# Kernel optimization log

Hardware: AMD Instinct MI355X
Metric: run time of the kernel (lower is better)

The kernel has to match this reference:

```python
import jax, jax.numpy as jnp
import numpy as np
import math

D_MODEL = 1024
NUM_HEADS = 16
HEAD_DIM = D_MODEL // NUM_HEADS


def setup_inputs() -> dict:
    key = jax.random.key(0)
    ks = jax.random.split(key, 10)
    B, Sq, Skv = 2, 2048, 2048
    s = 1.0 / math.sqrt(D_MODEL)
    return {
        "X": jax.random.normal(ks[0], (B, Skv, D_MODEL), jnp.float32),
        "y": jax.random.normal(ks[1], (B, Sq, D_MODEL), jnp.float32),
        "qW": jax.random.normal(ks[2], (D_MODEL, D_MODEL), jnp.float32) * s,
        "qB": jnp.zeros((D_MODEL,), jnp.float32),
        "kW": jax.random.normal(ks[3], (D_MODEL, D_MODEL), jnp.float32) * s,
        "kB": jnp.zeros((D_MODEL,), jnp.float32),
        "vW": jax.random.normal(ks[4], (D_MODEL, D_MODEL), jnp.float32) * s,
        "vB": jnp.zeros((D_MODEL,), jnp.float32),
        "oW": jax.random.normal(ks[5], (D_MODEL, D_MODEL), jnp.float32) * s,
        "oB": jnp.zeros((D_MODEL,), jnp.float32),
    }


def _split_heads(x):
    # (B, S, D) -> (B, H, S, dk)
    B, S, _ = x.shape
    return x.reshape(B, S, NUM_HEADS, HEAD_DIM).transpose(0, 2, 1, 3)


def reference(X, y, qW, qB, kW, kB, vW, vB, oW, oB):
    B = X.shape[0]
    q = _split_heads(y @ qW + qB)   # queries come from y (decoder)
    k = _split_heads(X @ kW + kB)   # keys/values from X (encoder)
    v = _split_heads(X @ vW + vB)
    scale = 1.0 / math.sqrt(HEAD_DIM)
    scores = jnp.einsum("bhqd,bhkd->bhqk", q, k) * scale
    weights = jax.nn.softmax(scores, axis=-1)
    attn = jnp.einsum("bhqk,bhkd->bhqd", weights, v)
    concat = attn.transpose(0, 2, 1, 3).reshape(B, -1, D_MODEL)
    return concat @ oW + oB
```

## Files before the change

kernel.cpp:

```cpp
#include <hip/hip_runtime.h>
#include <hip/hip_bf16.h>
#include <math.h>

typedef __hip_bfloat16 bf16;
typedef __bf16 nbf16;
typedef __bf16 bf16x8 __attribute__((ext_vector_type(8)));
typedef __bf16 bf16x4 __attribute__((ext_vector_type(4)));
typedef float f32x4 __attribute__((ext_vector_type(4)));

#define D_MODEL 1024
#define NHEAD   16
#define HDK     64
#define BATCH   2
#define SEQ     2048
#define QSZ     ((size_t)BATCH * SEQ * D_MODEL)
#define WSZ     ((size_t)D_MODEL * D_MODEL)

__global__ void detect_dtype(const unsigned short* __restrict__ x, int* flag) {
    __shared__ int cnt;
    if (threadIdx.x == 0) cnt = 0;
    __syncthreads();
    int local = 0;
    for (int i = threadIdx.x; i < 4096; i += 256) {
        const unsigned short v = x[i];
        const int e = (v >> 7) & 0xFF;
        if (v == 0 || (e >= 96 && e <= 141)) local++;
    }
    atomicAdd(&cnt, local);
    __syncthreads();
    if (threadIdx.x == 0) *flag = (cnt >= 3600) ? 1 : 0;
}

__device__ __forceinline__ float ldIn(const void* p, size_t i, int isbf16) {
    return isbf16 ? __bfloat162float(((const bf16*)p)[i])
                  : ((const float*)p)[i];
}

__device__ __forceinline__ void gload_lds16(const void* g, void* l) {
    __builtin_amdgcn_global_load_lds(
        (const __attribute__((address_space(1))) void*)g,
        (__attribute__((address_space(3))) void*)l, 16, 0, 0);
}

__global__ void tobf16_xy(const void* __restrict__ X, const void* __restrict__ Y,
                          nbf16* __restrict__ Xb, nbf16* __restrict__ Yb,
                          const int* __restrict__ flagp) {
    const int flag = *flagp;
    const int half = (int)(QSZ / 2048);
    const bool isX = blockIdx.x < half;
    const void* in = isX ? X : Y;
    nbf16* out     = isX ? Xb : Yb;
    const size_t i = ((size_t)(isX ? blockIdx.x : blockIdx.x - half) * 256 +
                      threadIdx.x) * 8;
    if (flag) {
        *(uint4*)(out + i) = *(const uint4*)((const nbf16*)in + i);
    } else {
        const float4 a = *(const float4*)((const float*)in + i);
        const float4 b = *(const float4*)((const float*)in + i + 4);
        bf16x8 v = {(nbf16)a.x, (nbf16)a.y, (nbf16)a.z, (nbf16)a.w,
                    (nbf16)b.x, (nbf16)b.y, (nbf16)b.z, (nbf16)b.w};
        *(bf16x8*)(out + i) = v;
    }
}

__global__ void wtrans4(const void* __restrict__ qW, const void* __restrict__ kW,
                        const void* __restrict__ vW, const void* __restrict__ oW,
                        nbf16* __restrict__ Wt3, nbf16* __restrict__ Wto,
                        const int* __restrict__ flagp) {
    const int flag = *flagp;
    const int z = blockIdx.z;
    const void* W = (z == 0) ? qW : (z == 1) ? kW : (z == 2) ? vW : oW;
    nbf16* Wt = (z == 3) ? Wto : Wt3 + (size_t)z * WSZ;

    __shared__ float T[64][65];
    const int k0 = blockIdx.x * 64, n0 = blockIdx.y * 64;
    #pragma unroll
    for (int i = 0; i < 16; ++i) {
        const int idx = threadIdx.x + i * 256;
        const int r = idx >> 6, c = idx & 63;
        T[r][c] = ldIn(W, (size_t)(k0 + r) * D_MODEL + n0 + c, flag);
    }
    __syncthreads();
    #pragma unroll
    for (int i = 0; i < 16; ++i) {
        const int idx = threadIdx.x + i * 256;
        const int n = idx >> 6, k = idx & 63;
        Wt[(size_t)(n0 + n) * D_MODEL + k0 + k] = (nbf16)T[k][n];
    }
}

#define STAGE128(Albuf, Blbuf, Aptr, Bptr, t)                                  \
{                                                                              \
    const int _k0 = (t) * 64;                                                  \
    _Pragma("unroll")                                                          \
    for (int i = 0; i < 4; ++i) {                                              \
        const int row = i * 32 + wid * 8 + (lane >> 3);                        \
        const int ss  = (lane & 7) ^ (row & 7);                                \
        gload_lds16((Aptr) + (size_t)row * D_MODEL + _k0 + ss * 8,             \
                    (nbf16*)(Albuf) + i * 2048 + wid * 512);                   \
        gload_lds16((Bptr) + (size_t)row * D_MODEL + _k0 + ss * 8,             \
                    (nbf16*)(Blbuf) + i * 2048 + wid * 512);                   \
    }                                                                          \
}

#define GEMM128_LOOP(Al, Bl)                                                   \
    const int NT = D_MODEL / 64;                                               \
    for (int t = 0; t < NT; ++t) {                                             \
        const int cur = t & 1;                                                 \
        if (t + 1 < NT)                                                        \
            STAGE128(&Al[cur ^ 1][0][0], &Bl[cur ^ 1][0][0], Am, Bm, t + 1);   \
        _Pragma("unroll")                                                      \
        for (int kk = 0; kk < 2; ++kk) {                                       \
            bf16x8 af[4], bfr[4];                                              \
            _Pragma("unroll")                                                  \
            for (int mi = 0; mi < 4; ++mi) {                                   \
                const int ar = wr * 64 + mi * 16 + l15;                        \
                const int sl = ((kk << 2) + lg) ^ (ar & 7);                    \
                af[mi] = *(const bf16x8*)((const nbf16*)&Al[cur][ar][0] + sl * 8); \
            }                                                                  \
            _Pragma("unroll")                                                  \
            for (int ni = 0; ni < 4; ++ni) {                                   \
                const int br = wc * 64 + ni * 16 + l15;                        \
                const int sl = ((kk << 2) + lg) ^ (br & 7);                    \
                bfr[ni] = *(const bf16x8*)((const nbf16*)&Bl[cur][br][0] + sl * 8); \
            }                                                                  \
            _Pragma("unroll")                                                  \
            for (int mi = 0; mi < 4; ++mi)                                     \
                _Pragma("unroll")                                              \
                for (int ni = 0; ni < 4; ++ni)                                 \
                    acc[mi][ni] = __builtin_amdgcn_mfma_f32_16x16x32_bf16(     \
                        af[mi], bfr[ni], acc[mi][ni], 0, 0, 0);                \
        }                                                                      \
        __syncthreads();                                                       \
    }

__global__ __launch_bounds__(256, 2) void proj_qkv(
        const nbf16* __restrict__ Xb, const nbf16* __restrict__ Yb,
        const nbf16* __restrict__ Wt3,
        const void* __restrict__ qB, const void* __restrict__ kB,
        const void* __restrict__ vB,
        nbf16* __restrict__ outq, const int* __restrict__ flagp) {
    __shared__ nbf16 Al[2][128][64];
    __shared__ nbf16 Bl[2][128][64];

    const int flag = *flagp;
    const int tid  = threadIdx.x;
    const int wid  = tid >> 6;
    const int lane = tid & 63;
    const int l15  = lane & 15;
    const int lg   = lane >> 4;
    const int wr   = wid >> 1;
    const int wc   = wid & 1;

    const int id = blockIdx.x;
    const int sw = (id & 7) * 96 + (id >> 3);
    const int m0  = (sw & 31) * 128;
    const int ng0 = (sw >> 5) * 128;

    const nbf16* A  = (ng0 < D_MODEL) ? Yb : Xb;
    const nbf16* Bm = Wt3 + (size_t)ng0 * D_MODEL;
    const nbf16* Am = A + (size_t)m0 * D_MODEL;

    f32x4 acc[4][4];
    #pragma unroll
    for (int mi = 0; mi < 4; ++mi)
        #pragma unroll
        for (int ni = 0; ni < 4; ++ni) acc[mi][ni] = (f32x4){0.f, 0.f, 0.f, 0.f};

    STAGE128(&Al[0][0][0], &Bl[0][0][0], Am, Bm, 0);
    __syncthreads();

    GEMM128_LOOP(Al, Bl)

    #pragma unroll
    for (int ni = 0; ni < 4; ++ni) {
        const int n  = ng0 + wc * 64 + ni * 16 + l15;
        const int wh = n >> 10;
        const int nl = n & 1023;
        const void* bp = (wh == 0) ? qB : (wh == 1) ? kB : vB;
        const float bias = ldIn(bp, (size_t)nl, flag);
        nbf16* outp = outq + (size_t)wh * QSZ;
        #pragma unroll
        for (int mi = 0; mi < 4; ++mi) {
            #pragma unroll
            for (int r = 0; r < 4; ++r) {
                const int m = m0 + wr * 64 + mi * 16 + lg * 4 + r;
                const float v = acc[mi][ni][r] + bias;
                const int b = m >> 11, s = m & (SEQ - 1);
                const int h = nl >> 6,  d = nl & (HDK - 1);
                outp[(((size_t)(b * NHEAD + h)) * SEQ + s) * HDK + d] = (nbf16)v;
            }
        }
    }
}

__global__ __launch_bounds__(256, 2) void proj_o(
        const nbf16* __restrict__ A, const nbf16* __restrict__ Wt,
        const void* __restrict__ Braw, void* __restrict__ Cout,
        const int* __restrict__ flagp) {
    __shared__ nbf16 Al[2][128][64];
    __shared__ nbf16 Bl[2][128][64];

    const int flag = *flagp;
    const int tid  = threadIdx.x;
    const int wid  = tid >> 6;
    const int lane = tid & 63;
    const int l15  = lane & 15;
    const int lg   = lane >> 4;
    const int wr   = wid >> 1;
    const int wc   = wid & 1;

    const int id = blockIdx.x;
    const int sw = (id & 7) * 32 + (id >> 3);
    const int m0 = (sw >> 3) * 128;
    const int n0 = (sw & 7) * 128;

    const nbf16* Am = A + (size_t)m0 * D_MODEL;
    const nbf16* Bm = Wt + (size_t)n0 * D_MODEL;

    f32x4 acc[4][4];
    #pragma unroll
    for (int mi = 0; mi < 4; ++mi)
        #pragma unroll
        for (int ni = 0; ni < 4; ++ni) acc[mi][ni] = (f32x4){0.f, 0.f, 0.f, 0.f};

    STAGE128(&Al[0][0][0], &Bl[0][0][0], Am, Bm, 0);
    __syncthreads();

    GEMM128_LOOP(Al, Bl)

    #pragma unroll
    for (int ni = 0; ni < 4; ++ni) {
        const int n = n0 + wc * 64 + ni * 16 + l15;
        const float bias = ldIn(Braw, (size_t)n, flag);
        #pragma unroll
        for (int mi = 0; mi < 4; ++mi) {
            #pragma unroll
            for (int r = 0; r < 4; ++r) {
                const int m = m0 + wr * 64 + mi * 16 + lg * 4 + r;
                const float v = acc[mi][ni][r] + bias;
                if (flag) ((bf16*)Cout)[(size_t)m * D_MODEL + n] = __float2bfloat16(v);
                else      ((float*)Cout)[(size_t)m * D_MODEL + n] = v;
            }
        }
    }
}

__global__ __launch_bounds__(256, 2) void attn_mfma(
        const nbf16* __restrict__ qg, const nbf16* __restrict__ kg,
        const nbf16* __restrict__ vg, nbf16* __restrict__ cg) {
    __shared__ nbf16 KL[2][64][64];
    __shared__ nbf16 VT[2][64][72];
    __shared__ nbf16 PB[4][32][72];

    const int tid  = threadIdx.x;
    const int wid  = tid >> 6;
    const int lane = tid & 63;
    const int l15  = lane & 15;
    const int lg   = lane >> 4;

    const int id = blockIdx.x;
    const int sw = (id & 7) * 64 + (id >> 3);
    const int bh = sw >> 4;
    const int qt = sw & 15;

    const nbf16* qb = qg + (size_t)bh * SEQ * HDK;
    const nbf16* kb = kg + (size_t)bh * SEQ * HDK;
    const nbf16* vb = vg + (size_t)bh * SEQ * HDK;

    const float SCf = 0.125f * 1.44269504088896340736f;

    const int qbase = qt * 128 + wid * 32;
    const nbf16* qpA = qb + (size_t)(qbase + l15) * HDK + lg * 8;
    const nbf16* qpB = qpA + 16 * HDK;
    bf16x8 qfA0 = *(const bf16x8*)qpA;
    bf16x8 qfA1 = *(const bf16x8*)(qpA + 32);
    bf16x8 qfB0 = *(const bf16x8*)qpB;
    bf16x8 qfB1 = *(const bf16x8*)(qpB + 32);
    #pragma unroll
    for (int j = 0; j < 8; ++j) {
        qfA0[j] = (nbf16)((float)qfA0[j] * SCf);
        qfA1[j] = (nbf16)((float)qfA1[j] * SCf);
        qfB0[j] = (nbf16)((float)qfB0[j] * SCf);
        qfB1[j] = (nbf16)((float)qfB1[j] * SCf);
    }

    const bf16x8 ones = {(nbf16)1.f, (nbf16)1.f, (nbf16)1.f, (nbf16)1.f,
                         (nbf16)1.f, (nbf16)1.f, (nbf16)1.f, (nbf16)1.f};

    const int g8 = (tid >> 5) * 8;
    const int p2 = (tid & 31) * 2;

    #define STAGEK(buf, t)                                                     \
    {                                                                          \
        _Pragma("unroll")                                                      \
        for (int i = 0; i < 2; ++i) {                                          \
            const int row = i * 32 + wid * 8 + (lane >> 3);                    \
            const int ss  = (lane & 7) ^ (row & 7);                            \
            gload_lds16(kb + (size_t)((t) * 64 + row) * HDK + ss * 8,          \
                        (nbf16*)&KL[buf][0][0] + i * 2048 + wid * 512);        \
        }                                                                      \
    }

    #define VLOAD(t)                                                           \
        a0 = *(const uint4*)(vb + (size_t)((t) * 64 + p2) * HDK + g8);         \
        a1 = *(const uint4*)(vb + (size_t)((t) * 64 + p2 + 1) * HDK + g8);

    #define VWRITE(buf)                                                        \
    {                                                                          \
        const unsigned short* e0 = (const unsigned short*)&a0;                 \
        const unsigned short* e1 = (const unsigned short*)&a1;                 \
        _Pragma("unroll")                                                      \
        for (int j = 0; j < 8; ++j)                                            \
            *(unsigned int*)&VT[buf][g8 + j][p2] =                             \
                (unsigned int)e0[j] | ((unsigned int)e1[j] << 16);             \
    }

    #define SOFTMAX(st, m2, o, osum, pbrow)                                    \
    do {                                                                       \
        float tmx[4];                                                          \
        _Pragma("unroll")                                                      \
        for (int s_ = 0; s_ < 4; ++s_)                                         \
            tmx[s_] = fmaxf(fmaxf(st[s_][0], st[s_][1]),                       \
                            fmaxf(st[s_][2], st[s_][3]));                      \
        float tm = fmaxf(fmaxf(tmx[0], tmx[1]), fmaxf(tmx[2], tmx[3]));        \
        tm = fmaxf(tm, __shfl_xor(tm, 16, 64));                                \
        tm = fmaxf(tm, __shfl_xor(tm, 32, 64));                                \
        const bool nresc = __all(tm - m2 <= 8.0f);                             \
        const float mref = nresc ? m2 : fmaxf(m2, tm);                         \
        _Pragma("unroll")                                                      \
        for (int s_ = 0; s_ < 4; ++s_) {                                       \
            const float p0 = exp2f(st[s_][0] - mref);                          \
            const float p1 = exp2f(st[s_][1] - mref);                          \
            const float p2_ = exp2f(st[s_][2] - mref);                         \
            const float p3 = exp2f(st[s_][3] - mref);                          \
            bf16x4 pk = {(nbf16)p0, (nbf16)p1, (nbf16)p2_, (nbf16)p3};         \
            *(bf16x4*)((pbrow) + s_ * 16 + lg * 4) = pk;                       \
        }                                                                      \
        if (!nresc) {                                                          \
            const float alpha = exp2f(m2 - mref);                              \
            m2 = mref;                                                         \
            float av[4];                                                       \
            _Pragma("unroll")                                                  \
            for (int r = 0; r < 4; ++r) av[r] = __shfl(alpha, lg * 4 + r, 64); \
            _Pragma("unroll")                                                  \
            for (int i = 0; i < 4; ++i)                                        \
                _Pragma("unroll")                                              \
                for (int r = 0; r < 4; ++r) o[i][r] *= av[r];                  \
            _Pragma("unroll")                                                  \
            for (int r = 0; r < 4; ++r) osum[r] *= av[r];                      \
        }                                                                      \
    } while (0)

    float m2A = -3.0e38f, m2B = -3.0e38f;
    f32x4 oA[4], oB[4], osumA, osumB;
    #pragma unroll
    for (int i = 0; i < 4; ++i) { oA[i] = (f32x4){0,0,0,0}; oB[i] = (f32x4){0,0,0,0}; }
    osumA = (f32x4){0, 0, 0, 0};
    osumB = (f32x4){0, 0, 0, 0};

    const int NT = SEQ / 64;

    {
        uint4 a0, a1;
        STAGEK(0, 0);
        VLOAD(0);
        VWRITE(0);
    }
    __syncthreads();

    for (int t = 0; t < NT; ++t) {
        const int cur = t & 1;
        uint4 a0, a1;
        if (t + 1 < NT) {
            STAGEK(cur ^ 1, t + 1);
            VLOAD(t + 1);
        }

        f32x4 stA[4], stB[4];
        __builtin_amdgcn_s_setprio(1);
        #pragma unroll
        for (int sub = 0; sub < 4; ++sub) {
            const int row = sub * 16 + l15;
            const int s0 = lg ^ (row & 7);
            const int s1 = (4 + lg) ^ (row & 7);
            const bf16x8 kf0 = *(const bf16x8*)((const nbf16*)&KL[cur][row][0] + s0 * 8);
            const bf16x8 kf1 = *(const bf16x8*)((const nbf16*)&KL[cur][row][0] + s1 * 8);
            f32x4 a = (f32x4){0,0,0,0};
            a = __builtin_amdgcn_mfma_f32_16x16x32_bf16(kf0, qfA0, a, 0, 0, 0);
            a = __builtin_amdgcn_mfma_f32_16x16x32_bf16(kf1, qfA1, a, 0, 0, 0);
            stA[sub] = a;
            f32x4 b = (f32x4){0,0,0,0};
            b = __builtin_amdgcn_mfma_f32_16x16x32_bf16(kf0, qfB0, b, 0, 0, 0);
            b = __builtin_amdgcn_mfma_f32_16x16x32_bf16(kf1, qfB1, b, 0, 0, 0);
            stB[sub] = b;
        }
        __builtin_amdgcn_s_setprio(0);

        SOFTMAX(stA, m2A, oA, osumA, &PB[wid][l15][0]);
        SOFTMAX(stB, m2B, oB, osumB, &PB[wid][16 + l15][0]);

        __asm__ volatile("s_waitcnt lgkmcnt(0)" ::: "memory");

        const bf16x8 pfA0 = *(const bf16x8*)&PB[wid][l15][lg * 8];
        const bf16x8 pfA1 = *(const bf16x8*)&PB[wid][l15][lg * 8 + 32];
        const bf16x8 pfB0 = *(const bf16x8*)&PB[wid][16 + l15][lg * 8];
        const bf16x8 pfB1 = *(const bf16x8*)&PB[wid][16 + l15][lg * 8 + 32];
        __builtin_amdgcn_s_setprio(1);
        #pragma unroll
        for (int db = 0; db < 4; ++db) {
            const bf16x8 vf0 = *(const bf16x8*)&VT[cur][db * 16 + l15][lg * 8];
            const bf16x8 vf1 = *(const bf16x8*)&VT[cur][db * 16 + l15][lg * 8 + 32];
            oA[db] = __builtin_amdgcn_mfma_f32_16x16x32_bf16(pfA0, vf0, oA[db], 0, 0, 0);
            oA[db] = __builtin_amdgcn_mfma_f32_16x16x32_bf16(pfA1, vf1, oA[db], 0, 0, 0);
            oB[db] = __builtin_amdgcn_mfma_f32_16x16x32_bf16(pfB0, vf0, oB[db], 0, 0, 0);
            oB[db] = __builtin_amdgcn_mfma_f32_16x16x32_bf16(pfB1, vf1, oB[db], 0, 0, 0);
        }
        osumA = __builtin_amdgcn_mfma_f32_16x16x32_bf16(pfA0, ones, osumA, 0, 0, 0);
        osumA = __builtin_amdgcn_mfma_f32_16x16x32_bf16(pfA1, ones, osumA, 0, 0, 0);
        osumB = __builtin_amdgcn_mfma_f32_16x16x32_bf16(pfB0, ones, osumB, 0, 0, 0);
        osumB = __builtin_amdgcn_mfma_f32_16x16x32_bf16(pfB1, ones, osumB, 0, 0, 0);
        __builtin_amdgcn_s_setprio(0);

        if (t + 1 < NT) VWRITE(cur ^ 1);
        __syncthreads();
    }

    const int b = bh >> 4, h = bh & 15;
    #pragma unroll
    for (int db = 0; db < 4; ++db) {
        #pragma unroll
        for (int r = 0; r < 4; ++r) {
            const int qA = qbase + lg * 4 + r;
            cg[((size_t)(b * SEQ + qA)) * D_MODEL + h * HDK + db * 16 + l15] =
                (nbf16)(oA[db][r] / osumA[r]);
            const int qB_ = qbase + 16 + lg * 4 + r;
            cg[((size_t)(b * SEQ + qB_)) * D_MODEL + h * HDK + db * 16 + l15] =
                (nbf16)(oB[db][r] / osumB[r]);
        }
    }
    #undef STAGEK
    #undef VLOAD
    #undef VWRITE
    #undef SOFTMAX
}

extern "C" void kernel_launch(void* const* d_in, const int* in_sizes, int n_in,
                              void* d_out, int out_size, void* d_ws, size_t ws_size,
                              hipStream_t stream) {
    const void* X  = d_in[0];
    const void* Y  = d_in[1];
    const void* qW = d_in[2];
    const void* qB = d_in[3];
    const void* kW = d_in[4];
    const void* kB = d_in[5];
    const void* vW = d_in[6];
    const void* vB = d_in[7];
    const void* oW = d_in[8];
    const void* oB = d_in[9];

    nbf16* ws = (nbf16*)d_ws;
    nbf16* qbuf = ws;
    nbf16* kbuf = qbuf + QSZ;
    nbf16* vbuf = kbuf + QSZ;
    nbf16* cbuf = vbuf + QSZ;
    nbf16* Xb   = cbuf + QSZ;
    nbf16* Yb   = Xb + QSZ;
    nbf16* Wt3  = Yb + QSZ;
    nbf16* Wto  = Wt3 + 3 * WSZ;
    int*   flag = (int*)(Wto + WSZ);

    detect_dtype<<<1, 256, 0, stream>>>((const unsigned short*)X, flag);

    tobf16_xy<<<(int)(2 * (QSZ / 2048)), 256, 0, stream>>>(X, Y, Xb, Yb, flag);

    wtrans4<<<dim3(16, 16, 4), 256, 0, stream>>>(qW, kW, vW, oW, Wt3, Wto, flag);

    proj_qkv<<<768, 256, 0, stream>>>(Xb, Yb, Wt3, qB, kB, vB, qbuf, flag);

    attn_mfma<<<512, 256, 0, stream>>>(qbuf, kbuf, vbuf, cbuf);

    proj_o<<<256, 256, 0, stream>>>(cbuf, Wto, oB, d_out, flag);
}
```

Measured before the change: 252.5 us.

## Merge conversion and weight-transpose kernels; XOR-swizzle attention LDS for V and P

Fuses the input bf16 conversion and the four weight transposes into one prep launch, removing a kernel launch and its tail. In the attention kernel it drops the padded LDS rows (72→64) for the V-transpose and P buffers and applies an XOR swizzle on writes and reads. The swizzle is meant to avoid LDS bank conflicts without padding and to shrink shared memory use. The risk is that the swizzle pattern is less conflict-free than the padding for some access patterns.

```diff
diff --git a/kernel.cpp b/kernel.cpp
--- a/kernel.cpp
+++ b/kernel.cpp
@@ -42,50 +42,51 @@
         (__attribute__((address_space(3))) void*)l, 16, 0, 0);
 }
 
-__global__ void tobf16_xy(const void* __restrict__ X, const void* __restrict__ Y,
-                          nbf16* __restrict__ Xb, nbf16* __restrict__ Yb,
-                          const int* __restrict__ flagp) {
+__global__ void prep(const void* __restrict__ X, const void* __restrict__ Y,
+                     const void* __restrict__ qW, const void* __restrict__ kW,
+                     const void* __restrict__ vW, const void* __restrict__ oW,
+                     nbf16* __restrict__ Xb, nbf16* __restrict__ Yb,
+                     nbf16* __restrict__ Wt3, nbf16* __restrict__ Wto,
+                     const int* __restrict__ flagp) {
     const int flag = *flagp;
-    const int half = (int)(QSZ / 2048);
-    const bool isX = blockIdx.x < half;
-    const void* in = isX ? X : Y;
-    nbf16* out     = isX ? Xb : Yb;
-    const size_t i = ((size_t)(isX ? blockIdx.x : blockIdx.x - half) * 256 +
-                      threadIdx.x) * 8;
-    if (flag) {
-        *(uint4*)(out + i) = *(const uint4*)((const nbf16*)in + i);
+    const int id = blockIdx.x;
+    if (id < 4096) {
+        const bool isX = id < 2048;
+        const void* in = isX ? X : Y;
+        nbf16* out     = isX ? Xb : Yb;
+        const size_t i = ((size_t)(isX ? id : id - 2048) * 256 +
+                          threadIdx.x) * 8;
+        if (flag) {
+            *(uint4*)(out + i) = *(const uint4*)((const nbf16*)in + i);
+        } else {
+            const float4 a = *(const float4*)((const float*)in + i);
+            const float4 b = *(const float4*)((const float*)in + i + 4);
+            bf16x8 v = {(nbf16)a.x, (nbf16)a.y, (nbf16)a.z, (nbf16)a.w,
+                        (nbf16)b.x, (nbf16)b.y, (nbf16)b.z, (nbf16)b.w};
+            *(bf16x8*)(out + i) = v;
+        }
     } else {
-        const float4 a = *(const float4*)((const float*)in + i);
-        const float4 b = *(const float4*)((const float*)in + i + 4);
-        bf16x8 v = {(nbf16)a.x, (nbf16)a.y, (nbf16)a.z, (nbf16)a.w,
-                    (nbf16)b.x, (nbf16)b.y, (nbf16)b.z, (nbf16)b.w};
-        *(bf16x8*)(out + i) = v;
-    }
-}
-
-__global__ void wtrans4(const void* __restrict__ qW, const void* __restrict__ kW,
-                        const void* __restrict__ vW, const void* __restrict__ oW,
-                        nbf16* __restrict__ Wt3, nbf16* __restrict__ Wto,
-                        const int* __restrict__ flagp) {
-    const int flag = *flagp;
-    const int z = blockIdx.z;
-    const void* W = (z == 0) ? qW : (z == 1) ? kW : (z == 2) ? vW : oW;
-    nbf16* Wt = (z == 3) ? Wto : Wt3 + (size_t)z * WSZ;
-
-    __shared__ float T[64][65];
-    const int k0 = blockIdx.x * 64, n0 = blockIdx.y * 64;
-    #pragma unroll
-    for (int i = 0; i < 16; ++i) {
-        const int idx = threadIdx.x + i * 256;
-        const int r = idx >> 6, c = idx & 63;
-        T[r][c] = ldIn(W, (size_t)(k0 + r) * D_MODEL + n0 + c, flag);
-    }
-    __syncthreads();
-    #pragma unroll
-    for (int i = 0; i < 16; ++i) {
-        const int idx = threadIdx.x + i * 256;
-        const int n = idx >> 6, k = idx & 63;
-        Wt[(size_t)(n0 + n) * D_MODEL + k0 + k] = (nbf16)T[k][n];
+        const int t = id - 4096;
+        const int z = t >> 8;
+        const int tile = t & 255;
+        const void* W = (z == 0) ? qW : (z == 1) ? kW : (z == 2) ? vW : oW;
+        nbf16* Wt = (z == 3) ? Wto : Wt3 + (size_t)z * WSZ;
+
+        __shared__ float T[64][65];
+        const int k0 = (tile & 15) * 64, n0 = (tile >> 4) * 64;
+        #pragma unroll
+        for (int i = 0; i < 16; ++i) {
+            const int idx = threadIdx.x + i * 256;
+            const int r = idx >> 6, c = idx & 63;
+            T[r][c] = ldIn(W, (size_t)(k0 + r) * D_MODEL + n0 + c, flag);
+        }
+        __syncthreads();
+        #pragma unroll
+        for (int i = 0; i < 16; ++i) {
+            const int idx = threadIdx.x + i * 256;
+            const int n = idx >> 6, k = idx & 63;
+            Wt[(size_t)(n0 + n) * D_MODEL + k0 + k] = (nbf16)T[k][n];
+        }
     }
 }
 
@@ -250,8 +251,8 @@
         const nbf16* __restrict__ qg, const nbf16* __restrict__ kg,
         const nbf16* __restrict__ vg, nbf16* __restrict__ cg) {
     __shared__ nbf16 KL[2][64][64];
-    __shared__ nbf16 VT[2][64][72];
-    __shared__ nbf16 PB[4][32][72];
+    __shared__ nbf16 VT[2][64][64];
+    __shared__ nbf16 PB[4][32][64];
 
     const int tid  = threadIdx.x;
     const int wid  = tid >> 6;
@@ -290,6 +291,9 @@
 
     const int g8 = (tid >> 5) * 8;
     const int p2 = (tid & 31) * 2;
+
+    const int swz0 = (lg * 8)      ^ ((l15 & 7) << 3);
+    const int swz1 = (lg * 8 + 32) ^ ((l15 & 7) << 3);
 
     #define STAGEK(buf, t)                                                     \
     {                                                                          \
@@ -312,7 +316,7 @@
         const unsigned short* e1 = (const unsigned short*)&a1;                 \
         _Pragma("unroll")                                                      \
         for (int j = 0; j < 8; ++j)                                            \
-            *(unsigned int*)&VT[buf][g8 + j][p2] =                             \
+            *(unsigned int*)&VT[buf][g8 + j][p2 ^ (j << 3)] =                  \
                 (unsigned int)e0[j] | ((unsigned int)e1[j] << 16);             \
     }
 
@@ -335,7 +339,7 @@
             const float p2_ = exp2f(st[s_][2] - mref);                         \
             const float p3 = exp2f(st[s_][3] - mref);                          \
             bf16x4 pk = {(nbf16)p0, (nbf16)p1, (nbf16)p2_, (nbf16)p3};         \
-            *(bf16x4*)((pbrow) + s_ * 16 + lg * 4) = pk;                       \
+            *(bf16x4*)((pbrow) + ((s_ * 16 + lg * 4) ^ ((l15 & 7) << 3))) = pk;\
         }                                                                      \
         if (!nresc) {                                                          \
             const float alpha = exp2f(m2 - mref);                              \
@@ -402,15 +406,18 @@
 
         __asm__ volatile("s_waitcnt lgkmcnt(0)" ::: "memory");
 
-        const bf16x8 pfA0 = *(const bf16x8*)&PB[wid][l15][lg * 8];
-        const bf16x8 pfA1 = *(const bf16x8*)&PB[wid][l15][lg * 8 + 32];
-        const bf16x8 pfB0 = *(const bf16x8*)&PB[wid][16 + l15][lg * 8];
-        const bf16x8 pfB1 = *(const bf16x8*)&PB[wid][16 + l15][lg * 8 + 32];
+        const nbf16* pbA = &PB[wid][l15][0];
+        const nbf16* pbB = &PB[wid][16 + l15][0];
+        const bf16x8 pfA0 = *(const bf16x8*)(pbA + swz0);
+        const bf16x8 pfA1 = *(const bf16x8*)(pbA + swz1);
+        const bf16x8 pfB0 = *(const bf16x8*)(pbB + swz0);
+        const bf16x8 pfB1 = *(const bf16x8*)(pbB + swz1);
         __builtin_amdgcn_s_setprio(1);
         #pragma unroll
         for (int db = 0; db < 4; ++db) {
-            const bf16x8 vf0 = *(const bf16x8*)&VT[cur][db * 16 + l15][lg * 8];
-            const bf16x8 vf1 = *(const bf16x8*)&VT[cur][db * 16 + l15][lg * 8 + 32];
+            const nbf16* vr = &VT[cur][db * 16 + l15][0];
+            const bf16x8 vf0 = *(const bf16x8*)(vr + swz0);
+            const bf16x8 vf1 = *(const bf16x8*)(vr + swz1);
             oA[db] = __builtin_amdgcn_mfma_f32_16x16x32_bf16(pfA0, vf0, oA[db], 0, 0, 0);
             oA[db] = __builtin_amdgcn_mfma_f32_16x16x32_bf16(pfA1, vf1, oA[db], 0, 0, 0);
             oB[db] = __builtin_amdgcn_mfma_f32_16x16x32_bf16(pfB0, vf0, oB[db], 0, 0, 0);
@@ -472,9 +479,7 @@
 
     detect_dtype<<<1, 256, 0, stream>>>((const unsigned short*)X, flag);
 
-    tobf16_xy<<<(int)(2 * (QSZ / 2048)), 256, 0, stream>>>(X, Y, Xb, Yb, flag);
-
-    wtrans4<<<dim3(16, 16, 4), 256, 0, stream>>>(qW, kW, vW, oW, Wt3, Wto, flag);
+    prep<<<5120, 256, 0, stream>>>(X, Y, qW, kW, vW, oW, Xb, Yb, Wt3, Wto, flag);
 
     proj_qkv<<<768, 256, 0, stream>>>(Xb, Yb, Wt3, qB, kB, vB, qbuf, flag);
 
```

Measured after the change: 250.8 us. About the same (-0.7%).
